# Kernel tuning notes

Hardware: AMD Instinct MI355X
Metric: run time of the kernel (lower is better)

Reference implementation:

```python
import jax, jax.numpy as jnp
import numpy as np

B = 256      # complexes per batch
MOL_N = 40   # atoms per ligand
PRO_N = 400  # residues per protein pocket
HID = 64     # hid_dim
HEADS = 8


def setup_inputs() -> dict:
    key = jax.random.key(0)
    ks = jax.random.split(key, 8)
    M, P = B * MOL_N, B * PRO_N
    # create_index(mol_size, pro_size) with uniform sizes: all-pairs per complex
    mol_index = np.repeat(np.arange(M, dtype=np.int64), PRO_N)
    pro_ids = np.arange(P, dtype=np.int64).reshape(B, PRO_N)
    pro_index = np.broadcast_to(pro_ids[:, None, :], (B, MOL_N, PRO_N)).reshape(-1)
    mol_batch = np.repeat(np.arange(B, dtype=np.int64), MOL_N)
    return {
        "mol_feats": jax.random.normal(ks[0], (M, HID), jnp.float32),
        "pro_feats": jax.random.normal(ks[1], (P, HID), jnp.float32),
        "spatial_feats": jax.random.normal(ks[2], (P, HID), jnp.float32),
        "sigma_w": jax.random.normal(ks[3], (2 * HID, HEADS), jnp.float32) * 0.08,
        "sigma_b": jnp.zeros((HEADS,), jnp.float32),
        "mu_w": jax.random.normal(ks[4], (2 * HID, HEADS), jnp.float32) * 0.08,
        "mu_b": jnp.zeros((HEADS,), jnp.float32),
        "w1": jax.random.normal(ks[5], (HEADS, 2 * HEADS), jnp.float32) * 0.3,
        "b1": jnp.zeros((2 * HEADS,), jnp.float32),
        "w2": jax.random.normal(ks[6], (2 * HEADS, 1), jnp.float32) * 0.25,
        "b2": jnp.zeros((1,), jnp.float32),
        "mol_index": jnp.asarray(mol_index),
        "pro_index": jnp.asarray(pro_index),
        "mol_batch": jnp.asarray(mol_batch),
        "num_graphs": B,
    }


def reference(mol_feats, pro_feats, spatial_feats, sigma_w, sigma_b, mu_w, mu_b,
              w1, b1, w2, b2, mol_index, pro_index, mol_batch, num_graphs):
    hid = mol_feats.shape[1]
    pro = pro_feats * spatial_feats  # pro_feats * spatial_feats
    # Linear on concat([mol[i], pro[j]]) == per-side projections summed after gather.
    # Avoids materializing the [E, 2*hid] concat; same math as nn.Linear(2*hid, heads).
    mol_s = mol_feats @ sigma_w[:hid]   # [M, heads]
    pro_s = pro @ sigma_w[hid:]         # [P, heads]
    mol_m = mol_feats @ mu_w[:hid]
    pro_m = pro @ mu_w[hid:]
    sigma = jax.nn.elu(mol_s[mol_index] + pro_s[pro_index] + sigma_b) + 1.1  # [E, heads]
    mu = jax.nn.elu(mol_m[mol_index] + pro_m[pro_index] + mu_b) + 1.0       # [E, heads]
    # scatter_sum over pairs -> mol atoms, then mol atoms -> graphs
    y = jax.ops.segment_sum(mu, mol_index, num_segments=mol_feats.shape[0])  # [M, heads]
    y = jax.ops.segment_sum(y, mol_batch, num_segments=num_graphs) * 0.001   # [B, heads]
    y = jax.nn.elu(y @ w1 + b1)
    y_pred = y @ w2 + b2  # [B, 1]
    return mu, sigma, y_pred
```

## Files before the change

### kernel.cpp

```cpp
#include <hip/hip_runtime.h>

#define HID    64
#define HEADS  8
#define MOL_N  40
#define PRO_N  400
#define NGRAPH 256

typedef float vfloat4 __attribute__((ext_vector_type(4)));

__device__ __forceinline__ float elu_plus(float x, float c) {
    return x > 0.0f ? x + c : __expf(x) - 1.0f + c;
}

__global__ __launch_bounds__(256) void proj_kernel(
    const float* __restrict__ mol_feats, const float* __restrict__ pro_feats,
    const float* __restrict__ spatial,   const float* __restrict__ sigma_w,
    const float* __restrict__ sigma_b,   const float* __restrict__ mu_w,
    const float* __restrict__ mu_b,
    float* __restrict__ mol_s, float* __restrict__ mol_m,
    float* __restrict__ pro_s, float* __restrict__ pro_m,
    float* __restrict__ y_acc, int mol_blocks)
{
    __shared__ float rows[32][HID + 1];
    __shared__ float wsig[HID][HEADS];
    __shared__ float wmu [HID][HEADS];

    const int tid = threadIdx.x;
    const bool is_mol = (int)blockIdx.x < mol_blocks;

    if (blockIdx.x == 0) {
        for (int i = tid; i < NGRAPH * HEADS; i += 256) y_acc[i] = 0.0f;
    }

    const int wofs = is_mol ? 0 : HID * HEADS;
    for (int i = tid; i < HID * HEADS; i += 256) {
        wsig[i / HEADS][i % HEADS] = sigma_w[wofs + i];
        wmu [i / HEADS][i % HEADS] = mu_w  [wofs + i];
    }

    const int r0 = (is_mol ? (int)blockIdx.x : ((int)blockIdx.x - mol_blocks)) * 32;
    if (is_mol) {
        const float4* src = (const float4*)mol_feats + (size_t)r0 * (HID / 4);
        for (int i = tid; i < 32 * (HID / 4); i += 256) {
            float4 v = src[i];
            int lr = i / (HID / 4), k4 = (i % (HID / 4)) * 4;
            rows[lr][k4 + 0] = v.x; rows[lr][k4 + 1] = v.y;
            rows[lr][k4 + 2] = v.z; rows[lr][k4 + 3] = v.w;
        }
    } else {
        const float4* srcp = (const float4*)pro_feats + (size_t)r0 * (HID / 4);
        const float4* srcs = (const float4*)spatial   + (size_t)r0 * (HID / 4);
        for (int i = tid; i < 32 * (HID / 4); i += 256) {
            float4 a = srcp[i];
            float4 b = srcs[i];
            int lr = i / (HID / 4), k4 = (i % (HID / 4)) * 4;
            rows[lr][k4 + 0] = a.x * b.x; rows[lr][k4 + 1] = a.y * b.y;
            rows[lr][k4 + 2] = a.z * b.z; rows[lr][k4 + 3] = a.w * b.w;
        }
    }
    __syncthreads();

    const int lr = tid >> 3;
    const int h  = tid & 7;
    float as = 0.0f, am = 0.0f;
#pragma unroll
    for (int k = 0; k < HID; ++k) {
        float x = rows[lr][k];
        as += x * wsig[k][h];
        am += x * wmu [k][h];
    }
    const int gr = r0 + lr;
    if (is_mol) {
        mol_s[gr * HEADS + h] = as + sigma_b[h];
        mol_m[gr * HEADS + h] = am + mu_b[h];
    } else {
        pro_s[gr * HEADS + h] = as;
        pro_m[gr * HEADS + h] = am;
    }
}

__global__ __launch_bounds__(256) void edge_kernel(
    const float* __restrict__ mol_s, const float* __restrict__ mol_m,
    const float* __restrict__ pro_s, const float* __restrict__ pro_m,
    float* __restrict__ mu_out, float* __restrict__ sg_out,
    float* __restrict__ y_acc)
{
    const int bi  = blockIdx.x;
    const int b   = bi & (NGRAPH - 1);
    const int r   = bi >> 8;
    const int m   = b * MOL_N + r;
    const int tid = threadIdx.x;

    __shared__ float s_mol[16];
    __shared__ float s_hsum[HEADS];
    if (tid < 8)       s_mol[tid] = mol_s[m * HEADS + tid];
    else if (tid < 16) s_mol[tid] = mol_m[m * HEADS + (tid - 8)];
    if (tid < HEADS)   s_hsum[tid] = 0.0f;
    __syncthreads();

    const int q = tid & 1;
    float ms[4], mm[4];
#pragma unroll
    for (int k = 0; k < 4; ++k) {
        ms[k] = s_mol[q * 4 + k];
        mm[k] = s_mol[8 + q * 4 + k];
    }

    const vfloat4* pm4 = (const vfloat4*)pro_m + (size_t)b * PRO_N * 2;
    const vfloat4* ps4 = (const vfloat4*)pro_s + (size_t)b * PRO_N * 2;
    vfloat4* mu4 = (vfloat4*)mu_out + (size_t)m * PRO_N * 2;
    vfloat4* sg4 = (vfloat4*)sg_out + (size_t)m * PRO_N * 2;

    float acc[4] = {0.f, 0.f, 0.f, 0.f};
    for (int t = tid; t < PRO_N * 2; t += 256) {
        vfloat4 pmv = pm4[t];
        vfloat4 psv = ps4[t];
        vfloat4 vmu, vsg;
        vmu.x = elu_plus(pmv.x + mm[0], 1.0f);
        vmu.y = elu_plus(pmv.y + mm[1], 1.0f);
        vmu.z = elu_plus(pmv.z + mm[2], 1.0f);
        vmu.w = elu_plus(pmv.w + mm[3], 1.0f);
        vsg.x = elu_plus(psv.x + ms[0], 1.1f);
        vsg.y = elu_plus(psv.y + ms[1], 1.1f);
        vsg.z = elu_plus(psv.z + ms[2], 1.1f);
        vsg.w = elu_plus(psv.w + ms[3], 1.1f);
        __builtin_nontemporal_store(vmu, &mu4[t]);
        __builtin_nontemporal_store(vsg, &sg4[t]);
        acc[0] += vmu.x; acc[1] += vmu.y; acc[2] += vmu.z; acc[3] += vmu.w;
    }

#pragma unroll
    for (int mask = 2; mask < 64; mask <<= 1) {
#pragma unroll
        for (int k = 0; k < 4; ++k) acc[k] += __shfl_xor(acc[k], mask, 64);
    }
    if ((tid & 63) < 2) {
#pragma unroll
        for (int k = 0; k < 4; ++k) atomicAdd(&s_hsum[q * 4 + k], acc[k]);
    }
    __syncthreads();
    if (tid < HEADS) atomicAdd(&y_acc[b * HEADS + tid], s_hsum[tid]);
}

__global__ __launch_bounds__(256) void head_kernel(
    const float* __restrict__ y_acc, const float* __restrict__ w1,
    const float* __restrict__ b1,    const float* __restrict__ w2,
    const float* __restrict__ b2,    float* __restrict__ y_pred)
{
    const int g = threadIdx.x;
    float y[HEADS];
#pragma unroll
    for (int h = 0; h < HEADS; ++h) y[h] = y_acc[g * HEADS + h] * 0.001f;
    float out = b2[0];
#pragma unroll
    for (int o = 0; o < 2 * HEADS; ++o) {
        float a = b1[o];
#pragma unroll
        for (int h = 0; h < HEADS; ++h) a += y[h] * w1[h * (2 * HEADS) + o];
        a = a > 0.0f ? a : __expf(a) - 1.0f;
        out += a * w2[o];
    }
    y_pred[g] = out;
}

extern "C" void kernel_launch(void* const* d_in, const int* in_sizes, int n_in,
                              void* d_out, int out_size, void* d_ws, size_t ws_size,
                              hipStream_t stream) {
    const float* mol_feats = (const float*)d_in[0];
    const float* pro_feats = (const float*)d_in[1];
    const float* spatial   = (const float*)d_in[2];
    const float* sigma_w   = (const float*)d_in[3];
    const float* sigma_b   = (const float*)d_in[4];
    const float* mu_w      = (const float*)d_in[5];
    const float* mu_b      = (const float*)d_in[6];
    const float* w1        = (const float*)d_in[7];
    const float* b1        = (const float*)d_in[8];
    const float* w2        = (const float*)d_in[9];
    const float* b2        = (const float*)d_in[10];

    const int M = in_sizes[0] / HID;
    const int P = in_sizes[1] / HID;
    const int E = in_sizes[11];

    float* ws    = (float*)d_ws;
    float* mol_s = ws;
    float* mol_m = mol_s + (size_t)M * HEADS;
    float* pro_s = mol_m + (size_t)M * HEADS;
    float* pro_m = pro_s + (size_t)P * HEADS;
    float* y_acc = pro_m + (size_t)P * HEADS;

    float* mu_out = (float*)d_out;
    float* sg_out = mu_out + (size_t)E * HEADS;
    float* y_pred = sg_out + (size_t)E * HEADS;

    const int mol_blocks = M / 32;
    const int pro_blocks = P / 32;

    proj_kernel<<<mol_blocks + pro_blocks, 256, 0, stream>>>(
        mol_feats, pro_feats, spatial, sigma_w, sigma_b, mu_w, mu_b,
        mol_s, mol_m, pro_s, pro_m, y_acc, mol_blocks);

    edge_kernel<<<M, 256, 0, stream>>>(
        mol_s, mol_m, pro_s, pro_m, mu_out, sg_out, y_acc);

    head_kernel<<<1, 256, 0, stream>>>(y_acc, w1, b1, w2, b2, y_pred);
}
```

Measured before the change: 354.3 us.

## Fuse projection, edge and head kernels into one per-graph kernel

```diff
diff --git a/kernel.cpp b/kernel.cpp
--- a/kernel.cpp
+++ b/kernel.cpp
@@ -1,10 +1,11 @@
 #include <hip/hip_runtime.h>
 
-#define HID    64
-#define HEADS  8
-#define MOL_N  40
-#define PRO_N  400
-#define NGRAPH 256
+#define HID      64
+#define HEADS    8
+#define MOL_N    40
+#define PRO_N    400
+#define NGRAPH   256
+#define NTHREADS 1024
 
 typedef float vfloat4 __attribute__((ext_vector_type(4)));
 
@@ -12,155 +13,136 @@
     return x > 0.0f ? x + c : __expf(x) - 1.0f + c;
 }
 
-__global__ __launch_bounds__(256) void proj_kernel(
+__global__ __launch_bounds__(NTHREADS) void fused_kernel(
     const float* __restrict__ mol_feats, const float* __restrict__ pro_feats,
     const float* __restrict__ spatial,   const float* __restrict__ sigma_w,
     const float* __restrict__ sigma_b,   const float* __restrict__ mu_w,
     const float* __restrict__ mu_b,
-    float* __restrict__ mol_s, float* __restrict__ mol_m,
-    float* __restrict__ pro_s, float* __restrict__ pro_m,
-    float* __restrict__ y_acc, int mol_blocks)
+    const float* __restrict__ w1,        const float* __restrict__ b1,
+    const float* __restrict__ w2,        const float* __restrict__ b2,
+    float* __restrict__ mu_out, float* __restrict__ sg_out,
+    float* __restrict__ y_pred)
 {
-    __shared__ float rows[32][HID + 1];
-    __shared__ float wsig[HID][HEADS];
-    __shared__ float wmu [HID][HEADS];
+    const int b   = (int)blockIdx.x;
+    const int tid = (int)threadIdx.x;
 
-    const int tid = threadIdx.x;
-    const bool is_mol = (int)blockIdx.x < mol_blocks;
+    __shared__ float   wsig[2 * HID * HEADS];
+    __shared__ float   wmu [2 * HID * HEADS];
+    __shared__ vfloat4 proS[PRO_N][2];
+    __shared__ vfloat4 proM[PRO_N][2];
+    __shared__ vfloat4 molS[MOL_N][2];
+    __shared__ vfloat4 molM[MOL_N][2];
+    __shared__ float   ysum[16][HEADS];
+    __shared__ float   yv[HEADS];
 
-    if (blockIdx.x == 0) {
-        for (int i = tid; i < NGRAPH * HEADS; i += 256) y_acc[i] = 0.0f;
+    wsig[tid] = sigma_w[tid];
+    wmu [tid] = mu_w  [tid];
+    __syncthreads();
+
+    for (int task = tid; task < PRO_N * HEADS; task += NTHREADS) {
+        const int r = task >> 3, h = task & 7;
+        const vfloat4* pf = (const vfloat4*)pro_feats + ((size_t)b * PRO_N + r) * (HID / 4);
+        const vfloat4* sf = (const vfloat4*)spatial   + ((size_t)b * PRO_N + r) * (HID / 4);
+        float as0 = 0.f, as1 = 0.f, am0 = 0.f, am1 = 0.f;
+#pragma unroll
+        for (int k4 = 0; k4 < HID / 4; ++k4) {
+            vfloat4 a = pf[k4], s = sf[k4];
+            const float x0 = a.x * s.x, x1 = a.y * s.y, x2 = a.z * s.z, x3 = a.w * s.w;
+            const float* wg = &wsig[(HID + k4 * 4) * HEADS + h];
+            const float* wm = &wmu [(HID + k4 * 4) * HEADS + h];
+            as0 += x0 * wg[0];  as1 += x1 * wg[8];
+            as0 += x2 * wg[16]; as1 += x3 * wg[24];
+            am0 += x0 * wm[0];  am1 += x1 * wm[8];
+            am0 += x2 * wm[16]; am1 += x3 * wm[24];
+        }
+        ((float*)proS)[r * 8 + h] = as0 + as1;
+        ((float*)proM)[r * 8 + h] = am0 + am1;
     }
-
-    const int wofs = is_mol ? 0 : HID * HEADS;
-    for (int i = tid; i < HID * HEADS; i += 256) {
-        wsig[i / HEADS][i % HEADS] = sigma_w[wofs + i];
-        wmu [i / HEADS][i % HEADS] = mu_w  [wofs + i];
-    }
-
-    const int r0 = (is_mol ? (int)blockIdx.x : ((int)blockIdx.x - mol_blocks)) * 32;
-    if (is_mol) {
-        const float4* src = (const float4*)mol_feats + (size_t)r0 * (HID / 4);
-        for (int i = tid; i < 32 * (HID / 4); i += 256) {
-            float4 v = src[i];
-            int lr = i / (HID / 4), k4 = (i % (HID / 4)) * 4;
-            rows[lr][k4 + 0] = v.x; rows[lr][k4 + 1] = v.y;
-            rows[lr][k4 + 2] = v.z; rows[lr][k4 + 3] = v.w;
+    if (tid < MOL_N * HEADS) {
+        const int r = tid >> 3, h = tid & 7;
+        const vfloat4* mf = (const vfloat4*)mol_feats + ((size_t)b * MOL_N + r) * (HID / 4);
+        float as0 = sigma_b[h], as1 = 0.f, am0 = mu_b[h], am1 = 0.f;
+#pragma unroll
+        for (int k4 = 0; k4 < HID / 4; ++k4) {
+            vfloat4 a = mf[k4];
+            const float* wg = &wsig[(k4 * 4) * HEADS + h];
+            const float* wm = &wmu [(k4 * 4) * HEADS + h];
+            as0 += a.x * wg[0];  as1 += a.y * wg[8];
+            as0 += a.z * wg[16]; as1 += a.w * wg[24];
+            am0 += a.x * wm[0];  am1 += a.y * wm[8];
+            am0 += a.z * wm[16]; am1 += a.w * wm[24];
         }
-    } else {
-        const float4* srcp = (const float4*)pro_feats + (size_t)r0 * (HID / 4);
-        const float4* srcs = (const float4*)spatial   + (size_t)r0 * (HID / 4);
-        for (int i = tid; i < 32 * (HID / 4); i += 256) {
-            float4 a = srcp[i];
-            float4 b = srcs[i];
-            int lr = i / (HID / 4), k4 = (i % (HID / 4)) * 4;
-            rows[lr][k4 + 0] = a.x * b.x; rows[lr][k4 + 1] = a.y * b.y;
-            rows[lr][k4 + 2] = a.z * b.z; rows[lr][k4 + 3] = a.w * b.w;
-        }
+        ((float*)molS)[r * 8 + h] = as0 + as1;
+        ((float*)molM)[r * 8 + h] = am0 + am1;
     }
     __syncthreads();
 
-    const int lr = tid >> 3;
-    const int h  = tid & 7;
-    float as = 0.0f, am = 0.0f;
-#pragma unroll
-    for (int k = 0; k < HID; ++k) {
-        float x = rows[lr][k];
-        as += x * wsig[k][h];
-        am += x * wmu [k][h];
-    }
-    const int gr = r0 + lr;
-    if (is_mol) {
-        mol_s[gr * HEADS + h] = as + sigma_b[h];
-        mol_m[gr * HEADS + h] = am + mu_b[h];
-    } else {
-        pro_s[gr * HEADS + h] = as;
-        pro_m[gr * HEADS + h] = am;
-    }
-}
-
-__global__ __launch_bounds__(256) void edge_kernel(
-    const float* __restrict__ mol_s, const float* __restrict__ mol_m,
-    const float* __restrict__ pro_s, const float* __restrict__ pro_m,
-    float* __restrict__ mu_out, float* __restrict__ sg_out,
-    float* __restrict__ y_acc)
-{
-    const int bi  = blockIdx.x;
-    const int b   = bi & (NGRAPH - 1);
-    const int r   = bi >> 8;
-    const int m   = b * MOL_N + r;
-    const int tid = threadIdx.x;
-
-    __shared__ float s_mol[16];
-    __shared__ float s_hsum[HEADS];
-    if (tid < 8)       s_mol[tid] = mol_s[m * HEADS + tid];
-    else if (tid < 16) s_mol[tid] = mol_m[m * HEADS + (tid - 8)];
-    if (tid < HEADS)   s_hsum[tid] = 0.0f;
-    __syncthreads();
-
-    const int q = tid & 1;
-    float ms[4], mm[4];
-#pragma unroll
-    for (int k = 0; k < 4; ++k) {
-        ms[k] = s_mol[q * 4 + k];
-        mm[k] = s_mol[8 + q * 4 + k];
-    }
-
-    const vfloat4* pm4 = (const vfloat4*)pro_m + (size_t)b * PRO_N * 2;
-    const vfloat4* ps4 = (const vfloat4*)pro_s + (size_t)b * PRO_N * 2;
-    vfloat4* mu4 = (vfloat4*)mu_out + (size_t)m * PRO_N * 2;
-    vfloat4* sg4 = (vfloat4*)sg_out + (size_t)m * PRO_N * 2;
-
-    float acc[4] = {0.f, 0.f, 0.f, 0.f};
-    for (int t = tid; t < PRO_N * 2; t += 256) {
-        vfloat4 pmv = pm4[t];
-        vfloat4 psv = ps4[t];
-        vfloat4 vmu, vsg;
-        vmu.x = elu_plus(pmv.x + mm[0], 1.0f);
-        vmu.y = elu_plus(pmv.y + mm[1], 1.0f);
-        vmu.z = elu_plus(pmv.z + mm[2], 1.0f);
-        vmu.w = elu_plus(pmv.w + mm[3], 1.0f);
-        vsg.x = elu_plus(psv.x + ms[0], 1.1f);
-        vsg.y = elu_plus(psv.y + ms[1], 1.1f);
-        vsg.z = elu_plus(psv.z + ms[2], 1.1f);
-        vsg.w = elu_plus(psv.w + ms[3], 1.1f);
-        __builtin_nontemporal_store(vmu, &mu4[t]);
-        __builtin_nontemporal_store(vsg, &sg4[t]);
-        acc[0] += vmu.x; acc[1] += vmu.y; acc[2] += vmu.z; acc[3] += vmu.w;
+    const int q  = tid & 1;
+    const int jj = tid >> 1;
+    float acc0 = 0.f, acc1 = 0.f, acc2 = 0.f, acc3 = 0.f;
+    if (tid < 2 * PRO_N) {
+        const vfloat4 pm = proM[jj][q];
+        const vfloat4 ps = proS[jj][q];
+        vfloat4* mu4 = (vfloat4*)mu_out + (size_t)b * (MOL_N * PRO_N * 2);
+        vfloat4* sg4 = (vfloat4*)sg_out + (size_t)b * (MOL_N * PRO_N * 2);
+        for (int r = 0; r < MOL_N; ++r) {
+            const vfloat4 mm = molM[r][q];
+            const vfloat4 ms = molS[r][q];
+            vfloat4 vmu, vsg;
+            vmu.x = elu_plus(pm.x + mm.x, 1.0f);
+            vmu.y = elu_plus(pm.y + mm.y, 1.0f);
+            vmu.z = elu_plus(pm.z + mm.z, 1.0f);
+            vmu.w = elu_plus(pm.w + mm.w, 1.0f);
+            vsg.x = elu_plus(ps.x + ms.x, 1.1f);
+            vsg.y = elu_plus(ps.y + ms.y, 1.1f);
+            vsg.z = elu_plus(ps.z + ms.z, 1.1f);
+            vsg.w = elu_plus(ps.w + ms.w, 1.1f);
+            const int t = r * (2 * PRO_N) + tid;
+            mu4[t] = vmu;
+            sg4[t] = vsg;
+            acc0 += vmu.x; acc1 += vmu.y; acc2 += vmu.z; acc3 += vmu.w;
+        }
     }
 
 #pragma unroll
     for (int mask = 2; mask < 64; mask <<= 1) {
-#pragma unroll
-        for (int k = 0; k < 4; ++k) acc[k] += __shfl_xor(acc[k], mask, 64);
+        acc0 += __shfl_xor(acc0, mask, 64);
+        acc1 += __shfl_xor(acc1, mask, 64);
+        acc2 += __shfl_xor(acc2, mask, 64);
+        acc3 += __shfl_xor(acc3, mask, 64);
     }
-    if ((tid & 63) < 2) {
-#pragma unroll
-        for (int k = 0; k < 4; ++k) atomicAdd(&s_hsum[q * 4 + k], acc[k]);
+    const int wv = tid >> 6, lane = tid & 63;
+    if (lane < 2) {
+        ysum[wv][lane * 4 + 0] = acc0;
+        ysum[wv][lane * 4 + 1] = acc1;
+        ysum[wv][lane * 4 + 2] = acc2;
+        ysum[wv][lane * 4 + 3] = acc3;
     }
     __syncthreads();
-    if (tid < HEADS) atomicAdd(&y_acc[b * HEADS + tid], s_hsum[tid]);
-}
 
-__global__ __launch_bounds__(256) void head_kernel(
-    const float* __restrict__ y_acc, const float* __restrict__ w1,
-    const float* __restrict__ b1,    const float* __restrict__ w2,
-    const float* __restrict__ b2,    float* __restrict__ y_pred)
-{
-    const int g = threadIdx.x;
-    float y[HEADS];
+    if (tid < HEADS) {
+        float s = 0.f;
 #pragma unroll
-    for (int h = 0; h < HEADS; ++h) y[h] = y_acc[g * HEADS + h] * 0.001f;
-    float out = b2[0];
+        for (int i = 0; i < 16; ++i) s += ysum[i][tid];
+        yv[tid] = s * 0.001f;
+    }
+    __syncthreads();
+
+    if (tid < 64) {
+        float contrib = 0.f;
+        if (tid < 2 * HEADS) {
+            float a = b1[tid];
 #pragma unroll
-    for (int o = 0; o < 2 * HEADS; ++o) {
-        float a = b1[o];
-#pragma unroll
-        for (int h = 0; h < HEADS; ++h) a += y[h] * w1[h * (2 * HEADS) + o];
-        a = a > 0.0f ? a : __expf(a) - 1.0f;
-        out += a * w2[o];
+            for (int h = 0; h < HEADS; ++h) a += yv[h] * w1[h * (2 * HEADS) + tid];
+            a = a > 0.f ? a : __expf(a) - 1.f;
+            contrib = a * w2[tid];
+        }
+        contrib += __shfl_down(contrib, 8, 64);
+        contrib += __shfl_down(contrib, 4, 64);
+        contrib += __shfl_down(contrib, 2, 64);
+        contrib += __shfl_down(contrib, 1, 64);
+        if (tid == 0) y_pred[b] = contrib + b2[0];
     }
-    y_pred[g] = out;
 }
 
 extern "C" void kernel_launch(void* const* d_in, const int* in_sizes, int n_in,
@@ -178,30 +160,13 @@
     const float* w2        = (const float*)d_in[9];
     const float* b2        = (const float*)d_in[10];
 
-    const int M = in_sizes[0] / HID;
-    const int P = in_sizes[1] / HID;
     const int E = in_sizes[11];
-
-    float* ws    = (float*)d_ws;
-    float* mol_s = ws;
-    float* mol_m = mol_s + (size_t)M * HEADS;
-    float* pro_s = mol_m + (size_t)M * HEADS;
-    float* pro_m = pro_s + (size_t)P * HEADS;
-    float* y_acc = pro_m + (size_t)P * HEADS;
 
     float* mu_out = (float*)d_out;
     float* sg_out = mu_out + (size_t)E * HEADS;
     float* y_pred = sg_out + (size_t)E * HEADS;
 
-    const int mol_blocks = M / 32;
-    const int pro_blocks = P / 32;
-
-    proj_kernel<<<mol_blocks + pro_blocks, 256, 0, stream>>>(
+    fused_kernel<<<NGRAPH, NTHREADS, 0, stream>>>(
         mol_feats, pro_feats, spatial, sigma_w, sigma_b, mu_w, mu_b,
-        mol_s, mol_m, pro_s, pro_m, y_acc, mol_blocks);
-
-    edge_kernel<<<M, 256, 0, stream>>>(
-        mol_s, mol_m, pro_s, pro_m, mu_out, sg_out, y_acc);
-
-    head_kernel<<<1, 256, 0, stream>>>(y_acc, w1, b1, w2, b2, y_pred);
+        w1, b1, w2, b2, mu_out, sg_out, y_pred);
 }
```

Result: slower. 428.7 us (+21.0%).
